# Performance work log

Hardware: AMD Instinct MI355X
Metric: run time of the kernel (lower is better)

Reference implementation:

```python
import jax, jax.numpy as jnp
import numpy as np

N = 50000
E = 800000
IN_D, HID_D, EMB_D, K = 128, 128, 64, 16
ALPHA = 1.0
NEG_SLOPE = 0.2


def _l2norm(x, eps=1e-12):
    n = jnp.sqrt(jnp.sum(x * x, axis=1, keepdims=True))
    return x / jnp.maximum(n, eps)


def _gat(x, src, dst, W, a_src, a_dst, b, n_nodes):
    # PyG GATConv, heads=1: h = xW; e_ij = leakyrelu(a_src.h_j + a_dst.h_i)
    h = x @ W                                   # [N, D]
    al_s = h @ a_src                            # [N]
    al_d = h @ a_dst                            # [N]
    logits = jax.nn.leaky_relu(al_s[src] + al_d[dst], NEG_SLOPE)  # [E']
    m = jax.ops.segment_max(logits, dst, num_segments=n_nodes)
    ex = jnp.exp(logits - m[dst])
    denom = jax.ops.segment_sum(ex, dst, num_segments=n_nodes)
    alpha = ex / denom[dst]                     # softmax over incoming edges
    out = jax.ops.segment_sum(h[src] * alpha[:, None], dst, num_segments=n_nodes)
    return out + b


def _cluster_prob(z, cluster):
    z2 = jnp.sum(z * z, axis=1, keepdims=True)          # [N,1]
    c2 = jnp.sum(cluster * cluster, axis=1)[None, :]    # [1,K]
    dist = z2 + c2 - 2.0 * (z @ cluster.T)              # [N,K]
    q = 1.0 / (1.0 + dist / ALPHA)
    q = (q + 1e-07) ** ((ALPHA + 1.0) / 2.0)
    return q / jnp.sum(q, axis=1, keepdims=True)


def setup_inputs() -> dict:
    key = jax.random.key(0)
    ks = jax.random.split(key, 20)
    d = {}
    d['x'] = jax.random.normal(ks[0], (N, IN_D), dtype=jnp.float32)
    d['edge_index'] = jax.random.randint(ks[1], (2, E), 0, N, dtype=jnp.int32)
    dims = [(IN_D, HID_D), (HID_D, EMB_D), (EMB_D, HID_D), (HID_D, IN_D)]
    for i, (di, do) in enumerate(dims):
        s = 1.0 / np.sqrt(di)
        d[f'W{i+1}'] = jax.random.normal(ks[2 + 4 * i], (di, do), dtype=jnp.float32) * s
        d[f'a{i+1}s'] = jax.random.normal(ks[3 + 4 * i], (do,), dtype=jnp.float32) * 0.1
        d[f'a{i+1}d'] = jax.random.normal(ks[4 + 4 * i], (do,), dtype=jnp.float32) * 0.1
        d[f'b{i+1}'] = jnp.zeros((do,), dtype=jnp.float32)
    d['cluster'] = jax.random.normal(ks[18], (K, EMB_D), dtype=jnp.float32) * 0.1
    return d


def reference(x, edge_index, W1, a1s, a1d, b1, W2, a2s, a2d, b2,
              W3, a3s, a3d, b3, W4, a4s, a4d, b4, cluster):
    # add self loops (PyG GATConv default)
    loop = jnp.arange(N, dtype=edge_index.dtype)
    src = jnp.concatenate([edge_index[0], loop])
    dst = jnp.concatenate([edge_index[1], loop])

    xn = _l2norm(x)
    h1 = jax.nn.relu(_gat(xn, src, dst, W1, a1s, a1d, b1, N))
    z = _gat(h1, src, dst, W2, a2s, a2d, b2, N)
    z = _l2norm(z)
    d1 = jax.nn.relu(_gat(z, src, dst, W3, a3s, a3d, b3, N))
    x_hat = _gat(d1, src, dst, W4, a4s, a4d, b4, N)
    q = _cluster_prob(z, cluster)
    return (z, x_hat, q)
```

## Files before the change

kernel.cpp:

```cpp
#include <hip/hip_runtime.h>

#define NN 50000
#define NE 800000
#define NBK 196
#define BCAP 8192
#define GEMM_GRID 391
#define WTOT 49152

typedef unsigned int uint;
typedef unsigned short ushort;
typedef __attribute__((ext_vector_type(8))) short short8v;
typedef __attribute__((ext_vector_type(4))) float float4v;

static __device__ __forceinline__ float waveReduceSum(float v) {
#pragma unroll
  for (int o = 32; o > 0; o >>= 1) v += __shfl_xor(v, o);
  return v;
}
static __device__ __forceinline__ float waveReduceMax(float v) {
#pragma unroll
  for (int o = 32; o > 0; o >>= 1) v = fmaxf(v, __shfl_xor(v, o));
  return v;
}
static __device__ __forceinline__ float bf_lo(uint u) { return __uint_as_float(u << 16); }
static __device__ __forceinline__ float bf_hi(uint u) { return __uint_as_float(u & 0xffff0000u); }
static __device__ __forceinline__ uint f2bf(float f) {
  uint u = __float_as_uint(f);
  return (u + 0x7fffu + ((u >> 16) & 1u)) >> 16;
}
static __device__ __forceinline__ int waveInclScan(int v, int lane) {
#pragma unroll
  for (int o = 1; o < 64; o <<= 1) {
    int u = __shfl_up(v, o);
    if (lane >= o) v += u;
  }
  return v;
}
static __device__ __forceinline__ void split8(const float* f, short8v& hi, short8v& lo) {
#pragma unroll
  for (int j = 0; j < 8; ++j) {
    uint h = f2bf(f[j]);
    hi[j] = (short)h;
    float hf = __uint_as_float(h << 16);
    lo[j] = (short)f2bf(f[j] - hf);
  }
}

__global__ void k_zero(int* bcnt) {
  if (threadIdx.x < NBK) bcnt[threadIdx.x] = 0;
}
__global__ __launch_bounds__(256) void k_bucket(
    const int* __restrict__ esrc, const int* __restrict__ edst,
    uint* __restrict__ ebuf, int* __restrict__ bcnt) {
  __shared__ int hist[NBK];
  __shared__ int gbase[NBK];
  int tid = threadIdx.x;
  for (int i = tid; i < NBK; i += 256) hist[i] = 0;
  __syncthreads();
  const int ET = NE + NN;
  int base = blockIdx.x * 4096;
  int myb[16];
  uint mypk[16];
#pragma unroll
  for (int j = 0; j < 16; ++j) {
    int e = base + j * 256 + tid;
    int s, d;
    if (e < NE) { s = esrc[e]; d = edst[e]; }
    else if (e < ET) { s = e - NE; d = s; }
    else { myb[j] = -1; continue; }
    int b = d >> 8;
    myb[j] = b;
    mypk[j] = (uint)s | ((uint)(d & 255) << 16);
    atomicAdd(&hist[b], 1);
  }
  __syncthreads();
  for (int i = tid; i < NBK; i += 256) {
    int h = hist[i];
    gbase[i] = h > 0 ? atomicAdd(&bcnt[i], h) : 0;
    hist[i] = 0;
  }
  __syncthreads();
#pragma unroll
  for (int j = 0; j < 16; ++j) {
    int b = myb[j];
    if (b < 0) continue;
    int r = atomicAdd(&hist[b], 1);
    int pos = gbase[b] + r;
    if (pos < BCAP) ebuf[(size_t)b * BCAP + pos] = mypk[j];
  }
}
__global__ __launch_bounds__(256) void k_csr(
    const uint* __restrict__ ebuf, const int* __restrict__ bcnt,
    int* __restrict__ indptr, int* __restrict__ srcs) {
  __shared__ int h[256];
  __shared__ int cur[256];
  __shared__ int wsm[4];
  __shared__ int bbs;
  int tid = threadIdx.x, b = blockIdx.x;
  int lane = tid & 63, wv = tid >> 6;
  int v = (tid < NBK) ? bcnt[tid] : 0;
  int inc = waveInclScan(v, lane);
  if (lane == 63) wsm[wv] = inc;
  __syncthreads();
  int woff = 0;
  for (int k = 0; k < wv; ++k) woff += wsm[k];
  if (tid == b) bbs = inc - v + woff;
  h[tid] = 0;
  __syncthreads();
  int bbase = bbs;
  int cnt = bcnt[b];
  const uint* eb = ebuf + (size_t)b * BCAP;
  for (int i = tid; i < cnt; i += 256) atomicAdd(&h[eb[i] >> 16], 1);
  __syncthreads();
  int hv = h[tid];
  int inc2 = waveInclScan(hv, lane);
  if (lane == 63) wsm[wv] = inc2;
  __syncthreads();
  int woff2 = 0;
  for (int k = 0; k < wv; ++k) woff2 += wsm[k];
  int nodeExcl = inc2 - hv + woff2;
  int node = b * 256 + tid;
  if (node < NN) indptr[node] = bbase + nodeExcl;
  if (node == NN - 1) indptr[NN] = bbase + nodeExcl + hv;
  cur[tid] = nodeExcl;
  __syncthreads();
  for (int i = tid; i < cnt; i += 256) {
    uint pk = eb[i];
    int r = atomicAdd(&cur[pk >> 16], 1);
    srcs[bbase + r] = (int)(pk & 0xffffu);
  }
}

__global__ void k_wprep(const float* __restrict__ W1, const float* __restrict__ W2,
                        const float* __restrict__ W3, const float* __restrict__ W4,
                        ushort* __restrict__ hi, ushort* __restrict__ lo) {
  int i = blockIdx.x * 256 + threadIdx.x;
  if (i >= WTOT) return;
  const float* W; int DO, base;
  if (i < 16384)      { W = W1; DO = 128; base = 0; }
  else if (i < 24576) { W = W2; DO = 64;  base = 16384; }
  else if (i < 32768) { W = W3; DO = 128; base = 24576; }
  else                { W = W4; DO = 128; base = 32768; }
  int idx = i - base;
  int k = idx / DO, col = idx % DO;
  float w = W[idx];
  uint h = f2bf(w);
  float hf = __uint_as_float(h << 16);
  uint l2 = f2bf(w - hf);
  int CT = DO >> 4;
  int fo = base + (((k >> 5) * CT + (col >> 4)) * 64 + ((col & 15) | (((k >> 3) & 3) << 4))) * 8 + (k & 7);
  hi[fo] = (ushort)h;
  lo[fo] = (ushort)l2;
}

template <int K, int DO, bool NORM>
__global__ __launch_bounds__(256) void k_gemm_mfma(
    const float* __restrict__ X, const ushort* __restrict__ Whi,
    const ushort* __restrict__ Wlo,
    const float* __restrict__ avs, const float* __restrict__ avd,
    ushort* __restrict__ H, float* __restrict__ als, float* __restrict__ ald, int n) {
  constexpr int KS = K / 32, CT = DO / 16;
  constexpr int W4N = K * DO / 8;
  __shared__ ushort sWhi[K * DO];
  __shared__ ushort sWlo[K * DO];
  __shared__ float sas[DO], sad[DO];
  int tid = threadIdx.x;
  for (int i = tid; i < DO; i += 256) { sas[i] = avs[i]; sad[i] = avd[i]; }
  {
    const uint4* ghi = (const uint4*)Whi;
    const uint4* glo = (const uint4*)Wlo;
    uint4* shi = (uint4*)sWhi;
    uint4* slo = (uint4*)sWlo;
    for (int i = tid; i < W4N; i += 256) { shi[i] = ghi[i]; slo[i] = glo[i]; }
  }
  __syncthreads();
  int lane = tid & 63, wv = tid >> 6;
  int ntiles = (n + 63) >> 6;
  for (int tile = blockIdx.x; tile < ntiles; tile += gridDim.x) {
    int r0 = tile * 64 + wv * 16;
    if (r0 >= n) continue;
    int row = r0 + (lane & 15);
    int sub = lane >> 4;
    const float* xrow = X + (size_t)row * K;
    float xr[KS][8];
#pragma unroll
    for (int s = 0; s < KS; ++s) {
      *(float4*)&xr[s][0] = *(const float4*)(xrow + s * 32 + sub * 8);
      *(float4*)&xr[s][4] = *(const float4*)(xrow + s * 32 + sub * 8 + 4);
    }
    if (NORM) {
      float ss = 0.f;
#pragma unroll
      for (int s = 0; s < KS; ++s)
#pragma unroll
        for (int j = 0; j < 8; ++j) ss += xr[s][j] * xr[s][j];
      ss += __shfl_xor(ss, 16);
      ss += __shfl_xor(ss, 32);
      float sc = 1.0f / fmaxf(sqrtf(ss), 1e-12f);
#pragma unroll
      for (int s = 0; s < KS; ++s)
#pragma unroll
        for (int j = 0; j < 8; ++j) xr[s][j] *= sc;
    }
    float4v acc[CT];
#pragma unroll
    for (int c = 0; c < CT; ++c) acc[c] = (float4v){0.f, 0.f, 0.f, 0.f};
#pragma unroll
    for (int s = 0; s < KS; ++s) {
      short8v ahi, alo;
      split8(xr[s], ahi, alo);
#pragma unroll
      for (int c = 0; c < CT; ++c) {
        short8v bhi = *(const short8v*)&sWhi[(s * CT + c) * 512 + lane * 8];
        short8v blo = *(const short8v*)&sWlo[(s * CT + c) * 512 + lane * 8];
        acc[c] = __builtin_amdgcn_mfma_f32_16x16x32_bf16(ahi, bhi, acc[c], 0, 0, 0);
        acc[c] = __builtin_amdgcn_mfma_f32_16x16x32_bf16(ahi, blo, acc[c], 0, 0, 0);
        acc[c] = __builtin_amdgcn_mfma_f32_16x16x32_bf16(alo, bhi, acc[c], 0, 0, 0);
      }
    }
    int rbase = r0 + (sub << 2);
    float alsp[4] = {0.f, 0.f, 0.f, 0.f};
    float aldp[4] = {0.f, 0.f, 0.f, 0.f};
#pragma unroll
    for (int c = 0; c < CT; ++c) {
      int col = (c << 4) + (lane & 15);
      float as_ = sas[col], ad_ = sad[col];
#pragma unroll
      for (int j = 0; j < 4; ++j) {
        float v = acc[c][j];
        alsp[j] += v * as_;
        aldp[j] += v * ad_;
        uint bv = f2bf(v);
        uint nb = __shfl_xor(bv, 1);
        if (!(lane & 1)) {
          *(uint*)&H[(size_t)(rbase + j) * DO + col] = bv | (nb << 16);
        }
      }
    }
#pragma unroll
    for (int j = 0; j < 4; ++j) {
      float vs = alsp[j], vd = aldp[j];
#pragma unroll
      for (int o = 1; o < 16; o <<= 1) { vs += __shfl_xor(vs, o); vd += __shfl_xor(vd, o); }
      if ((lane & 15) == 0) { als[rbase + j] = vs; ald[rbase + j] = vd; }
    }
  }
}

template <int D, int MODE>
__global__ __launch_bounds__(256) void k_attn_aggr(
    const int* __restrict__ indptr, const int* __restrict__ srcs,
    const float* __restrict__ als, const float* __restrict__ ald,
    const ushort* __restrict__ H, const float* __restrict__ bias,
    float* __restrict__ out, const float* __restrict__ cluster,
    float* __restrict__ qout, int n) {
  constexpr int CAP = 256;
  __shared__ float slg[4][CAP];
  __shared__ int ssrc[4][CAP];
  __shared__ float scl[MODE == 2 ? 1024 : 4];
  __shared__ float sz[4][MODE == 2 ? 64 : 4];
  int w = (blockIdx.x * blockDim.x + threadIdx.x) >> 6;
  int l = threadIdx.x & 63;
  int wv = threadIdx.x >> 6;
  if (MODE == 2) {
    for (int i = threadIdx.x; i < 1024; i += 256) scl[i] = cluster[i];
    __syncthreads();
  }
  if (w >= n) return;
  int s0 = indptr[w], s1 = indptr[w + 1];
  int deg = s1 - s0;
  float ad = ald[w];
  float inv;
  float ax = 0.f, ay = 0.f, az = 0.f, aw = 0.f;
  const uint2* Hr = (const uint2*)H;
  if (deg <= CAP) {
    float mx = -1e30f;
    for (int t = l; t < deg; t += 64) {
      int s = srcs[s0 + t];
      float v = als[s] + ad;
      v = v >= 0.f ? v : 0.2f * v;
      ssrc[wv][t] = s;
      slg[wv][t] = v;
      mx = fmaxf(mx, v);
    }
    mx = waveReduceMax(mx);
    float sum = 0.f;
    for (int t = l; t < deg; t += 64) {
      float e = __expf(slg[wv][t] - mx);
      slg[wv][t] = e;
      sum += e;
    }
    sum = waveReduceSum(sum);
    inv = 1.0f / sum;
    if (D == 128) {
      int g = l >> 5, j = l & 31;
      int i = 0;
      for (; i + 16 <= deg; i += 16) {
        float p[8]; int e[8]; uint2 u[8];
#pragma unroll
        for (int r = 0; r < 8; ++r) { int idx = i + 2 * r + g; p[r] = slg[wv][idx]; e[r] = ssrc[wv][idx]; }
#pragma unroll
        for (int r = 0; r < 8; ++r) u[r] = Hr[(size_t)e[r] * 32 + j];
#pragma unroll
        for (int r = 0; r < 8; ++r) {
          ax += p[r] * bf_lo(u[r].x); ay += p[r] * bf_hi(u[r].x);
          az += p[r] * bf_lo(u[r].y); aw += p[r] * bf_hi(u[r].y);
        }
      }
      for (; i + 8 <= deg; i += 8) {
        float p[4]; int e[4]; uint2 u[4];
#pragma unroll
        for (int r = 0; r < 4; ++r) { int idx = i + 2 * r + g; p[r] = slg[wv][idx]; e[r] = ssrc[wv][idx]; }
#pragma unroll
        for (int r = 0; r < 4; ++r) u[r] = Hr[(size_t)e[r] * 32 + j];
#pragma unroll
        for (int r = 0; r < 4; ++r) {
          ax += p[r] * bf_lo(u[r].x); ay += p[r] * bf_hi(u[r].x);
          az += p[r] * bf_lo(u[r].y); aw += p[r] * bf_hi(u[r].y);
        }
      }
      for (; i < deg; i += 2) {
        int idx = i + g;
        if (idx < deg) {
          float p = slg[wv][idx];
          uint2 u = Hr[(size_t)ssrc[wv][idx] * 32 + j];
          ax += p * bf_lo(u.x); ay += p * bf_hi(u.x);
          az += p * bf_lo(u.y); aw += p * bf_hi(u.y);
        }
      }
    } else {
      int g = l >> 4, j = l & 15;
      int i = 0;
      for (; i + 32 <= deg; i += 32) {
        float p[8]; int e[8]; uint2 u[8];
#pragma unroll
        for (int r = 0; r < 8; ++r) { int idx = i + 4 * r + g; p[r] = slg[wv][idx]; e[r] = ssrc[wv][idx]; }
#pragma unroll
        for (int r = 0; r < 8; ++r) u[r] = Hr[(size_t)e[r] * 16 + j];
#pragma unroll
        for (int r = 0; r < 8; ++r) {
          ax += p[r] * bf_lo(u[r].x); ay += p[r] * bf_hi(u[r].x);
          az += p[r] * bf_lo(u[r].y); aw += p[r] * bf_hi(u[r].y);
        }
      }
      for (; i + 16 <= deg; i += 16) {
        float p[4]; int e[4]; uint2 u[4];
#pragma unroll
        for (int r = 0; r < 4; ++r) { int idx = i + 4 * r + g; p[r] = slg[wv][idx]; e[r] = ssrc[wv][idx]; }
#pragma unroll
        for (int r = 0; r < 4; ++r) u[r] = Hr[(size_t)e[r] * 16 + j];
#pragma unroll
        for (int r = 0; r < 4; ++r) {
          ax += p[r] * bf_lo(u[r].x); ay += p[r] * bf_hi(u[r].x);
          az += p[r] * bf_lo(u[r].y); aw += p[r] * bf_hi(u[r].y);
        }
      }
      for (; i < deg; i += 4) {
        int idx = i + g;
        if (idx < deg) {
          float p = slg[wv][idx];
          uint2 u = Hr[(size_t)ssrc[wv][idx] * 16 + j];
          ax += p * bf_lo(u.x); ay += p * bf_hi(u.x);
          az += p * bf_lo(u.y); aw += p * bf_hi(u.y);
        }
      }
    }
  } else {
    float mx = -1e30f;
    for (int t = l; t < deg; t += 64) {
      int s = srcs[s0 + t];
      float v = als[s] + ad;
      v = v >= 0.f ? v : 0.2f * v;
      mx = fmaxf(mx, v);
    }
    mx = waveReduceMax(mx);
    float sum = 0.f;
    for (int t = l; t < deg; t += 64) {
      int s = srcs[s0 + t];
      float v = als[s] + ad;
      v = v >= 0.f ? v : 0.2f * v;
      sum += __expf(v - mx);
    }
    sum = waveReduceSum(sum);
    inv = 1.0f / sum;
    for (int base = 0; base < deg; base += 64) {
      int t = base + l;
      if (t < deg) {
        int s = srcs[s0 + t];
        float v = als[s] + ad;
        v = v >= 0.f ? v : 0.2f * v;
        ssrc[wv][l] = s;
        slg[wv][l] = __expf(v - mx);
      }
      __builtin_amdgcn_wave_barrier();
      int m = min(64, deg - base);
      if (D == 128) {
        int g = l >> 5, j = l & 31;
        for (int i2 = g; i2 < m; i2 += 2) {
          float p = slg[wv][i2];
          uint2 u = Hr[(size_t)ssrc[wv][i2] * 32 + j];
          ax += p * bf_lo(u.x); ay += p * bf_hi(u.x);
          az += p * bf_lo(u.y); aw += p * bf_hi(u.y);
        }
      } else {
        int g = l >> 4, j = l & 15;
        for (int i2 = g; i2 < m; i2 += 4) {
          float p = slg[wv][i2];
          uint2 u = Hr[(size_t)ssrc[wv][i2] * 16 + j];
          ax += p * bf_lo(u.x); ay += p * bf_hi(u.x);
          az += p * bf_lo(u.y); aw += p * bf_hi(u.y);
        }
      }
      __builtin_amdgcn_wave_barrier();
    }
  }
  if (D == 128) {
    ax += __shfl_xor(ax, 32); ay += __shfl_xor(ay, 32);
    az += __shfl_xor(az, 32); aw += __shfl_xor(aw, 32);
    if (l < 32) {
      float4 bv = ((const float4*)bias)[l];
      float v0 = ax * inv + bv.x, v1 = ay * inv + bv.y;
      float v2 = az * inv + bv.z, v3 = aw * inv + bv.w;
      if (MODE == 1) {
        v0 = fmaxf(v0, 0.f); v1 = fmaxf(v1, 0.f);
        v2 = fmaxf(v2, 0.f); v3 = fmaxf(v3, 0.f);
      }
      ((float4*)(out + (size_t)w * 128))[l] = make_float4(v0, v1, v2, v3);
    }
  } else {
    ax += __shfl_xor(ax, 16); ay += __shfl_xor(ay, 16);
    az += __shfl_xor(az, 16); aw += __shfl_xor(aw, 16);
    ax += __shfl_xor(ax, 32); ay += __shfl_xor(ay, 32);
    az += __shfl_xor(az, 32); aw += __shfl_xor(aw, 32);
    int j = l & 15;
    float4 bv = ((const float4*)bias)[j];
    float v0 = ax * inv + bv.x, v1 = ay * inv + bv.y;
    float v2 = az * inv + bv.z, v3 = aw * inv + bv.w;
    if (MODE == 2) {
      float ss = v0 * v0 + v1 * v1 + v2 * v2 + v3 * v3;
      ss += __shfl_xor(ss, 1); ss += __shfl_xor(ss, 2);
      ss += __shfl_xor(ss, 4); ss += __shfl_xor(ss, 8);
      float sc = 1.0f / fmaxf(sqrtf(ss), 1e-12f);
      v0 *= sc; v1 *= sc; v2 *= sc; v3 *= sc;
    }
    if (l < 16) ((float4*)(out + (size_t)w * 64))[j] = make_float4(v0, v1, v2, v3);
    if (MODE == 2) {
      if (l < 16) ((float4*)&sz[wv][0])[j] = make_float4(v0, v1, v2, v3);
      __builtin_amdgcn_wave_barrier();
      int kk = l >> 2, p = l & 3;
      const float* zr = &sz[wv][p * 16];
      const float* cr = &scl[kk * 64 + p * 16];
      float s = 0.f;
#pragma unroll
      for (int d = 0; d < 16; ++d) {
        float df = zr[d] - cr[d];
        s += df * df;
      }
      s += __shfl_xor(s, 1);
      s += __shfl_xor(s, 2);
      float qv = 1.0f / (1.0f + s) + 1e-7f;
      float t = qv;
      t += __shfl_xor(t, 4);
      t += __shfl_xor(t, 8);
      t += __shfl_xor(t, 16);
      t += __shfl_xor(t, 32);
      if (p == 0) qout[(size_t)w * 16 + kk] = qv / t;
    }
  }
}

extern "C" void kernel_launch(void* const* d_in, const int* in_sizes, int n_in,
                              void* d_out, int out_size, void* d_ws, size_t ws_size,
                              hipStream_t stream) {
  const float* x = (const float*)d_in[0];
  const int* ei = (const int*)d_in[1];
  const float* W1 = (const float*)d_in[2];
  const float* a1s = (const float*)d_in[3];
  const float* a1d = (const float*)d_in[4];
  const float* b1 = (const float*)d_in[5];
  const float* W2 = (const float*)d_in[6];
  const float* a2s = (const float*)d_in[7];
  const float* a2d = (const float*)d_in[8];
  const float* b2 = (const float*)d_in[9];
  const float* W3 = (const float*)d_in[10];
  const float* a3s = (const float*)d_in[11];
  const float* a3d = (const float*)d_in[12];
  const float* b3 = (const float*)d_in[13];
  const float* W4 = (const float*)d_in[14];
  const float* a4s = (const float*)d_in[15];
  const float* a4d = (const float*)d_in[16];
  const float* b4 = (const float*)d_in[17];
  const float* cluster = (const float*)d_in[18];

  float* out = (float*)d_out;
  float* z = out;
  float* xhat = out + (size_t)NN * 64;
  float* qout = xhat + (size_t)NN * 128;

  const int ET = NE + NN;
  float* wsf = (float*)d_ws;
  float* X = wsf;          wsf += (size_t)NN * 128;
  ushort* H = (ushort*)wsf; wsf += (size_t)NN * 64;
  float* als = wsf;        wsf += NN;
  float* ald = wsf;        wsf += NN;
  int* indptr = (int*)wsf; wsf += NN + 1;
  int* srcs = (int*)wsf;   wsf += ET;
  uint* ebuf = (uint*)wsf; wsf += (size_t)NBK * BCAP;
  int* bcnt = (int*)wsf;   wsf += NBK;
  ushort* wfhi = (ushort*)wsf; wsf += WTOT / 2;
  ushort* wflo = (ushort*)wsf; wsf += WTOT / 2;

  const int* esrc = ei;
  const int* edst = ei + NE;

  const int TB = 256;
  const int gW = (NN + 3) / 4;
  const int gB = (ET + 4095) / 4096;

  k_zero<<<1, 256, 0, stream>>>(bcnt);
  k_wprep<<<(WTOT + 255) / 256, 256, 0, stream>>>(W1, W2, W3, W4, wfhi, wflo);
  k_bucket<<<gB, 256, 0, stream>>>(esrc, edst, ebuf, bcnt);
  k_csr<<<NBK, 256, 0, stream>>>(ebuf, bcnt, indptr, srcs);

  k_gemm_mfma<128, 128, true><<<GEMM_GRID, 256, 0, stream>>>(
      x, wfhi, wflo, a1s, a1d, H, als, ald, NN);
  k_attn_aggr<128, 1><<<gW, TB, 0, stream>>>(indptr, srcs, als, ald, H, b1, X,
                                             nullptr, nullptr, NN);

  k_gemm_mfma<128, 64, false><<<GEMM_GRID, 256, 0, stream>>>(
      X, wfhi + 16384, wflo + 16384, a2s, a2d, H, als, ald, NN);
  k_attn_aggr<64, 2><<<gW, TB, 0, stream>>>(indptr, srcs, als, ald, H, b2, z,
                                            cluster, qout, NN);

  k_gemm_mfma<64, 128, false><<<GEMM_GRID, 256, 0, stream>>>(
      z, wfhi + 24576, wflo + 24576, a3s, a3d, H, als, ald, NN);
  k_attn_aggr<128, 1><<<gW, TB, 0, stream>>>(indptr, srcs, als, ald, H, b3, X,
                                             nullptr, nullptr, NN);

  k_gemm_mfma<128, 128, false><<<GEMM_GRID, 256, 0, stream>>>(
      X, wfhi + 32768, wflo + 32768, a4s, a4d, H, als, ald, NN);
  k_attn_aggr<128, 0><<<gW, TB, 0, stream>>>(indptr, srcs, als, ald, H, b4, xhat,
                                             nullptr, nullptr, NN);
}
```

Before: 254.1 us.

## Split attention aggregation into alpha, column-sliced aggregation and cluster kernels

Replaces the fused per-node softmax-plus-aggregation kernel with three kernels. One computes normalized edge softmax weights into a global buffer that reuses the edge bucket storage. One aggregates with each block handling a 32-column slice of four nodes. A separate kernel does the z L2-norm and cluster probabilities. The column split is meant to raise parallelism and cut register and shared-memory pressure in the gather. In exchange it adds extra launches and global round-trips of alpha, and re-reads srcs and indptr once per slice. It also folds the bucket-count zeroing into the weight-prep kernel, removing one launch.

Measured after the change: 477.9 us. 1.88x slower.

```diff
diff --git a/kernel.cpp b/kernel.cpp
--- a/kernel.cpp
+++ b/kernel.cpp
@@ -46,9 +46,6 @@
   }
 }
 
-__global__ void k_zero(int* bcnt) {
-  if (threadIdx.x < NBK) bcnt[threadIdx.x] = 0;
-}
 __global__ __launch_bounds__(256) void k_bucket(
     const int* __restrict__ esrc, const int* __restrict__ edst,
     uint* __restrict__ ebuf, int* __restrict__ bcnt) {
@@ -133,8 +130,10 @@
 
 __global__ void k_wprep(const float* __restrict__ W1, const float* __restrict__ W2,
                         const float* __restrict__ W3, const float* __restrict__ W4,
-                        ushort* __restrict__ hi, ushort* __restrict__ lo) {
+                        ushort* __restrict__ hi, ushort* __restrict__ lo,
+                        int* __restrict__ bcnt) {
   int i = blockIdx.x * 256 + threadIdx.x;
+  if (i < NBK) bcnt[i] = 0;
   if (i >= WTOT) return;
   const float* W; int DO, base;
   if (i < 16384)      { W = W1; DO = 128; base = 0; }
@@ -247,226 +246,120 @@
   }
 }
 
-template <int D, int MODE>
-__global__ __launch_bounds__(256) void k_attn_aggr(
+__global__ __launch_bounds__(256) void k_alpha(
     const int* __restrict__ indptr, const int* __restrict__ srcs,
     const float* __restrict__ als, const float* __restrict__ ald,
-    const ushort* __restrict__ H, const float* __restrict__ bias,
-    float* __restrict__ out, const float* __restrict__ cluster,
-    float* __restrict__ qout, int n) {
-  constexpr int CAP = 256;
-  __shared__ float slg[4][CAP];
-  __shared__ int ssrc[4][CAP];
-  __shared__ float scl[MODE == 2 ? 1024 : 4];
-  __shared__ float sz[4][MODE == 2 ? 64 : 4];
+    float* __restrict__ alpha, int n) {
   int w = (blockIdx.x * blockDim.x + threadIdx.x) >> 6;
   int l = threadIdx.x & 63;
-  int wv = threadIdx.x >> 6;
-  if (MODE == 2) {
-    for (int i = threadIdx.x; i < 1024; i += 256) scl[i] = cluster[i];
-    __syncthreads();
-  }
   if (w >= n) return;
   int s0 = indptr[w], s1 = indptr[w + 1];
-  int deg = s1 - s0;
   float ad = ald[w];
-  float inv;
-  float ax = 0.f, ay = 0.f, az = 0.f, aw = 0.f;
-  const uint2* Hr = (const uint2*)H;
-  if (deg <= CAP) {
-    float mx = -1e30f;
-    for (int t = l; t < deg; t += 64) {
-      int s = srcs[s0 + t];
-      float v = als[s] + ad;
-      v = v >= 0.f ? v : 0.2f * v;
-      ssrc[wv][t] = s;
-      slg[wv][t] = v;
-      mx = fmaxf(mx, v);
-    }
-    mx = waveReduceMax(mx);
-    float sum = 0.f;
-    for (int t = l; t < deg; t += 64) {
-      float e = __expf(slg[wv][t] - mx);
-      slg[wv][t] = e;
-      sum += e;
-    }
-    sum = waveReduceSum(sum);
-    inv = 1.0f / sum;
-    if (D == 128) {
-      int g = l >> 5, j = l & 31;
-      int i = 0;
-      for (; i + 16 <= deg; i += 16) {
-        float p[8]; int e[8]; uint2 u[8];
-#pragma unroll
-        for (int r = 0; r < 8; ++r) { int idx = i + 2 * r + g; p[r] = slg[wv][idx]; e[r] = ssrc[wv][idx]; }
-#pragma unroll
-        for (int r = 0; r < 8; ++r) u[r] = Hr[(size_t)e[r] * 32 + j];
-#pragma unroll
-        for (int r = 0; r < 8; ++r) {
-          ax += p[r] * bf_lo(u[r].x); ay += p[r] * bf_hi(u[r].x);
-          az += p[r] * bf_lo(u[r].y); aw += p[r] * bf_hi(u[r].y);
-        }
-      }
-      for (; i + 8 <= deg; i += 8) {
-        float p[4]; int e[4]; uint2 u[4];
-#pragma unroll
-        for (int r = 0; r < 4; ++r) { int idx = i + 2 * r + g; p[r] = slg[wv][idx]; e[r] = ssrc[wv][idx]; }
-#pragma unroll
-        for (int r = 0; r < 4; ++r) u[r] = Hr[(size_t)e[r] * 32 + j];
-#pragma unroll
-        for (int r = 0; r < 4; ++r) {
-          ax += p[r] * bf_lo(u[r].x); ay += p[r] * bf_hi(u[r].x);
-          az += p[r] * bf_lo(u[r].y); aw += p[r] * bf_hi(u[r].y);
-        }
-      }
-      for (; i < deg; i += 2) {
-        int idx = i + g;
-        if (idx < deg) {
-          float p = slg[wv][idx];
-          uint2 u = Hr[(size_t)ssrc[wv][idx] * 32 + j];
-          ax += p * bf_lo(u.x); ay += p * bf_hi(u.x);
-          az += p * bf_lo(u.y); aw += p * bf_hi(u.y);
-        }
-      }
-    } else {
-      int g = l >> 4, j = l & 15;
-      int i = 0;
-      for (; i + 32 <= deg; i += 32) {
-        float p[8]; int e[8]; uint2 u[8];
-#pragma unroll
-        for (int r = 0; r < 8; ++r) { int idx = i + 4 * r + g; p[r] = slg[wv][idx]; e[r] = ssrc[wv][idx]; }
-#pragma unroll
-        for (int r = 0; r < 8; ++r) u[r] = Hr[(size_t)e[r] * 16 + j];
-#pragma unroll
-        for (int r = 0; r < 8; ++r) {
-          ax += p[r] * bf_lo(u[r].x); ay += p[r] * bf_hi(u[r].x);
-          az += p[r] * bf_lo(u[r].y); aw += p[r] * bf_hi(u[r].y);
-        }
-      }
-      for (; i + 16 <= deg; i += 16) {
-        float p[4]; int e[4]; uint2 u[4];
-#pragma unroll
-        for (int r = 0; r < 4; ++r) { int idx = i + 4 * r + g; p[r] = slg[wv][idx]; e[r] = ssrc[wv][idx]; }
-#pragma unroll
-        for (int r = 0; r < 4; ++r) u[r] = Hr[(size_t)e[r] * 16 + j];
-#pragma unroll
-        for (int r = 0; r < 4; ++r) {
-          ax += p[r] * bf_lo(u[r].x); ay += p[r] * bf_hi(u[r].x);
-          az += p[r] * bf_lo(u[r].y); aw += p[r] * bf_hi(u[r].y);
-        }
-      }
-      for (; i < deg; i += 4) {
-        int idx = i + g;
-        if (idx < deg) {
-          float p = slg[wv][idx];
-          uint2 u = Hr[(size_t)ssrc[wv][idx] * 16 + j];
-          ax += p * bf_lo(u.x); ay += p * bf_hi(u.x);
-          az += p * bf_lo(u.y); aw += p * bf_hi(u.y);
-        }
-      }
-    }
-  } else {
-    float mx = -1e30f;
-    for (int t = l; t < deg; t += 64) {
-      int s = srcs[s0 + t];
-      float v = als[s] + ad;
-      v = v >= 0.f ? v : 0.2f * v;
-      mx = fmaxf(mx, v);
-    }
-    mx = waveReduceMax(mx);
-    float sum = 0.f;
-    for (int t = l; t < deg; t += 64) {
-      int s = srcs[s0 + t];
-      float v = als[s] + ad;
-      v = v >= 0.f ? v : 0.2f * v;
-      sum += __expf(v - mx);
-    }
-    sum = waveReduceSum(sum);
-    inv = 1.0f / sum;
-    for (int base = 0; base < deg; base += 64) {
-      int t = base + l;
-      if (t < deg) {
-        int s = srcs[s0 + t];
-        float v = als[s] + ad;
-        v = v >= 0.f ? v : 0.2f * v;
-        ssrc[wv][l] = s;
-        slg[wv][l] = __expf(v - mx);
-      }
-      __builtin_amdgcn_wave_barrier();
-      int m = min(64, deg - base);
-      if (D == 128) {
-        int g = l >> 5, j = l & 31;
-        for (int i2 = g; i2 < m; i2 += 2) {
-          float p = slg[wv][i2];
-          uint2 u = Hr[(size_t)ssrc[wv][i2] * 32 + j];
-          ax += p * bf_lo(u.x); ay += p * bf_hi(u.x);
-          az += p * bf_lo(u.y); aw += p * bf_hi(u.y);
-        }
-      } else {
-        int g = l >> 4, j = l & 15;
-        for (int i2 = g; i2 < m; i2 += 4) {
-          float p = slg[wv][i2];
-          uint2 u = Hr[(size_t)ssrc[wv][i2] * 16 + j];
-          ax += p * bf_lo(u.x); ay += p * bf_hi(u.x);
-          az += p * bf_lo(u.y); aw += p * bf_hi(u.y);
-        }
-      }
-      __builtin_amdgcn_wave_barrier();
-    }
-  }
-  if (D == 128) {
-    ax += __shfl_xor(ax, 32); ay += __shfl_xor(ay, 32);
-    az += __shfl_xor(az, 32); aw += __shfl_xor(aw, 32);
-    if (l < 32) {
-      float4 bv = ((const float4*)bias)[l];
-      float v0 = ax * inv + bv.x, v1 = ay * inv + bv.y;
-      float v2 = az * inv + bv.z, v3 = aw * inv + bv.w;
-      if (MODE == 1) {
-        v0 = fmaxf(v0, 0.f); v1 = fmaxf(v1, 0.f);
-        v2 = fmaxf(v2, 0.f); v3 = fmaxf(v3, 0.f);
-      }
-      ((float4*)(out + (size_t)w * 128))[l] = make_float4(v0, v1, v2, v3);
-    }
-  } else {
-    ax += __shfl_xor(ax, 16); ay += __shfl_xor(ay, 16);
-    az += __shfl_xor(az, 16); aw += __shfl_xor(aw, 16);
-    ax += __shfl_xor(ax, 32); ay += __shfl_xor(ay, 32);
-    az += __shfl_xor(az, 32); aw += __shfl_xor(aw, 32);
-    int j = l & 15;
-    float4 bv = ((const float4*)bias)[j];
-    float v0 = ax * inv + bv.x, v1 = ay * inv + bv.y;
-    float v2 = az * inv + bv.z, v3 = aw * inv + bv.w;
-    if (MODE == 2) {
-      float ss = v0 * v0 + v1 * v1 + v2 * v2 + v3 * v3;
-      ss += __shfl_xor(ss, 1); ss += __shfl_xor(ss, 2);
-      ss += __shfl_xor(ss, 4); ss += __shfl_xor(ss, 8);
-      float sc = 1.0f / fmaxf(sqrtf(ss), 1e-12f);
-      v0 *= sc; v1 *= sc; v2 *= sc; v3 *= sc;
-    }
-    if (l < 16) ((float4*)(out + (size_t)w * 64))[j] = make_float4(v0, v1, v2, v3);
-    if (MODE == 2) {
-      if (l < 16) ((float4*)&sz[wv][0])[j] = make_float4(v0, v1, v2, v3);
-      __builtin_amdgcn_wave_barrier();
-      int kk = l >> 2, p = l & 3;
-      const float* zr = &sz[wv][p * 16];
-      const float* cr = &scl[kk * 64 + p * 16];
-      float s = 0.f;
-#pragma unroll
-      for (int d = 0; d < 16; ++d) {
-        float df = zr[d] - cr[d];
-        s += df * df;
-      }
-      s += __shfl_xor(s, 1);
-      s += __shfl_xor(s, 2);
-      float qv = 1.0f / (1.0f + s) + 1e-7f;
-      float t = qv;
-      t += __shfl_xor(t, 4);
-      t += __shfl_xor(t, 8);
-      t += __shfl_xor(t, 16);
-      t += __shfl_xor(t, 32);
-      if (p == 0) qout[(size_t)w * 16 + kk] = qv / t;
-    }
-  }
+  float mx = -1e30f;
+  for (int e = s0 + l; e < s1; e += 64) {
+    float v = als[srcs[e]] + ad;
+    v = v >= 0.f ? v : 0.2f * v;
+    alpha[e] = v;
+    mx = fmaxf(mx, v);
+  }
+  mx = waveReduceMax(mx);
+  float sum = 0.f;
+  for (int e = s0 + l; e < s1; e += 64) {
+    float ex = __expf(alpha[e] - mx);
+    alpha[e] = ex;
+    sum += ex;
+  }
+  sum = waveReduceSum(sum);
+  float inv = 1.0f / sum;
+  for (int e = s0 + l; e < s1; e += 64) alpha[e] *= inv;
+}
+
+template <int D, bool RELU>
+__global__ __launch_bounds__(256) void k_aggr_s(
+    const int* __restrict__ indptr, const int* __restrict__ srcs,
+    const float* __restrict__ alpha, const ushort* __restrict__ H,
+    const float* __restrict__ bias, float* __restrict__ out, int n) {
+  constexpr int NS = D / 32;
+  int s = blockIdx.x % NS;
+  int nb = blockIdx.x / NS;
+  int w = nb * 4 + (threadIdx.x >> 6);
+  if (w >= n) return;
+  int l = threadIdx.x & 63;
+  int g = l >> 4, j = l & 15;
+  int s0 = indptr[w], s1 = indptr[w + 1];
+  const uint* Hu = (const uint*)H;
+  uint base = (uint)(s * 16 + j);
+  float a0 = 0.f, a1 = 0.f;
+  int i = s0;
+  for (; i + 16 <= s1; i += 16) {
+    float p[4]; uint u[4];
+#pragma unroll
+    for (int r = 0; r < 4; ++r) {
+      int e = i + 4 * r + g;
+      p[r] = alpha[e];
+      u[r] = Hu[(size_t)srcs[e] * (D / 2) + base];
+    }
+#pragma unroll
+    for (int r = 0; r < 4; ++r) { a0 += p[r] * bf_lo(u[r]); a1 += p[r] * bf_hi(u[r]); }
+  }
+  for (; i < s1; i += 4) {
+    int e = i + g;
+    if (e < s1) {
+      float p = alpha[e];
+      uint u = Hu[(size_t)srcs[e] * (D / 2) + base];
+      a0 += p * bf_lo(u); a1 += p * bf_hi(u);
+    }
+  }
+  a0 += __shfl_xor(a0, 16); a1 += __shfl_xor(a1, 16);
+  a0 += __shfl_xor(a0, 32); a1 += __shfl_xor(a1, 32);
+  if (l < 16) {
+    float2 bv = ((const float2*)bias)[s * 16 + j];
+    float v0 = a0 + bv.x, v1 = a1 + bv.y;
+    if (RELU) { v0 = fmaxf(v0, 0.f); v1 = fmaxf(v1, 0.f); }
+    ((float2*)(out + (size_t)w * D))[s * 16 + j] = make_float2(v0, v1);
+  }
+}
+
+__global__ __launch_bounds__(256) void k_zq(float* __restrict__ z,
+                                            const float* __restrict__ cluster,
+                                            float* __restrict__ q, int n) {
+  __shared__ float scl[16][68];
+  __shared__ float sz[4][64];
+  int tid = threadIdx.x;
+  for (int i = tid; i < 1024; i += 256) scl[i >> 6][i & 63] = cluster[i];
+  __syncthreads();
+  int w = (blockIdx.x * 256 + tid) >> 6;
+  if (w >= n) return;
+  int l = tid & 63, wv = tid >> 6;
+  float4 zv = ((const float4*)(z + (size_t)w * 64))[l & 15];
+  float ss = zv.x * zv.x + zv.y * zv.y + zv.z * zv.z + zv.w * zv.w;
+  ss += __shfl_xor(ss, 1); ss += __shfl_xor(ss, 2);
+  ss += __shfl_xor(ss, 4); ss += __shfl_xor(ss, 8);
+  float sc = 1.0f / fmaxf(sqrtf(ss), 1e-12f);
+  float4 zn = make_float4(zv.x * sc, zv.y * sc, zv.z * sc, zv.w * sc);
+  if (l < 16) {
+    ((float4*)(z + (size_t)w * 64))[l] = zn;
+    ((float4*)&sz[wv][0])[l] = zn;
+  }
+  __builtin_amdgcn_wave_barrier();
+  int kk = l >> 2, p = l & 3;
+  const float* zr = &sz[wv][p * 16];
+  const float* cr = &scl[kk][p * 16];
+  float s = 0.f;
+#pragma unroll
+  for (int d = 0; d < 16; ++d) {
+    float df = zr[d] - cr[d];
+    s += df * df;
+  }
+  s += __shfl_xor(s, 1);
+  s += __shfl_xor(s, 2);
+  float qv = 1.0f / (1.0f + s) + 1e-7f;
+  float t = qv;
+  t += __shfl_xor(t, 4);
+  t += __shfl_xor(t, 8);
+  t += __shfl_xor(t, 16);
+  t += __shfl_xor(t, 32);
+  if (p == 0) q[(size_t)w * 16 + kk] = qv / t;
 }
 
 extern "C" void kernel_launch(void* const* d_in, const int* in_sizes, int n_in,
@@ -509,6 +402,7 @@
   int* bcnt = (int*)wsf;   wsf += NBK;
   ushort* wfhi = (ushort*)wsf; wsf += WTOT / 2;
   ushort* wflo = (ushort*)wsf; wsf += WTOT / 2;
+  float* alpha = (float*)ebuf;
 
   const int* esrc = ei;
   const int* edst = ei + NE;
@@ -517,28 +411,28 @@
   const int gW = (NN + 3) / 4;
   const int gB = (ET + 4095) / 4096;
 
-  k_zero<<<1, 256, 0, stream>>>(bcnt);
-  k_wprep<<<(WTOT + 255) / 256, 256, 0, stream>>>(W1, W2, W3, W4, wfhi, wflo);
+  k_wprep<<<(WTOT + 255) / 256, 256, 0, stream>>>(W1, W2, W3, W4, wfhi, wflo, bcnt);
   k_bucket<<<gB, 256, 0, stream>>>(esrc, edst, ebuf, bcnt);
   k_csr<<<NBK, 256, 0, stream>>>(ebuf, bcnt, indptr, srcs);
 
   k_gemm_mfma<128, 128, true><<<GEMM_GRID, 256, 0, stream>>>(
       x, wfhi, wflo, a1s, a1d, H, als, ald, NN);
-  k_attn_aggr<128, 1><<<gW, TB, 0, stream>>>(indptr, srcs, als, ald, H, b1, X,
-                                             nullptr, nullptr, NN);
+  k_alpha<<<gW, TB, 0, stream>>>(indptr, srcs, als, ald, alpha, NN);
+  k_aggr_s<128, true><<<gW * 4, TB, 0, stream>>>(indptr, srcs, alpha, H, b1, X, NN);
 
   k_gemm_mfma<128, 64, false><<<GEMM_GRID, 256, 0, stream>>>(
       X, wfhi + 16384, wflo + 16384, a2s, a2d, H, als, ald, NN);
-  k_attn_aggr<64, 2><<<gW, TB, 0, stream>>>(indptr, srcs, als, ald, H, b2, z,
-                                            cluster, qout, NN);
+  k_alpha<<<gW, TB, 0, stream>>>(indptr, srcs, als, ald, alpha, NN);
+  k_aggr_s<64, false><<<gW * 2, TB, 0, stream>>>(indptr, srcs, alpha, H, b2, z, NN);
+  k_zq<<<gW, TB, 0, stream>>>(z, cluster, qout, NN);
 
   k_gemm_mfma<64, 128, false><<<GEMM_GRID, 256, 0, stream>>>(
       z, wfhi + 24576, wflo + 24576, a3s, a3d, H, als, ald, NN);
-  k_attn_aggr<128, 1><<<gW, TB, 0, stream>>>(indptr, srcs, als, ald, H, b3, X,
-                                             nullptr, nullptr, NN);
+  k_alpha<<<gW, TB, 0, stream>>>(indptr, srcs, als, ald, alpha, NN);
+  k_aggr_s<128, true><<<gW * 4, TB, 0, stream>>>(indptr, srcs, alpha, H, b3, X, NN);
 
   k_gemm_mfma<128, 128, false><<<GEMM_GRID, 256, 0, stream>>>(
       X, wfhi + 32768, wflo + 32768, a4s, a4d, H, als, ald, NN);
-  k_attn_aggr<128, 0><<<gW, TB, 0, stream>>>(indptr, srcs, als, ald, H, b4, xhat,
-                                             nullptr, nullptr, NN);
-}
+  k_alpha<<<gW, TB, 0, stream>>>(indptr, srcs, als, ald, alpha, NN);
+  k_aggr_s<128, false><<<gW * 4, TB, 0, stream>>>(indptr, srcs, alpha, H, b4, xhat, NN);
+}
```
